# Kernel optimization log

Measured on AMD Instinct MI355X. Metric: run time of the kernel, lower is better.

## Reference

```python
import jax, jax.numpy as jnp
import numpy as np

B, N_LAT, N_CTX, DIM = 4, 512, 4096, 512
HEADS, DIM_HEAD = 8, 64
DIM_INNER = HEADS * DIM_HEAD  # 512


def setup_inputs() -> dict:
    key = jax.random.key(0)
    k1, k2, k3, k4, k5 = jax.random.split(key, 5)
    x = jax.random.normal(k1, (B, N_LAT, DIM), dtype=jnp.float32)
    context = jax.random.normal(k2, (B, N_CTX, DIM), dtype=jnp.float32)
    # eqx.nn.Linear weights have shape (out_features, in_features); scale ~ 1/sqrt(in)
    s = 1.0 / np.sqrt(DIM)
    Wq = jax.random.normal(k3, (DIM_INNER, DIM), dtype=jnp.float32) * s
    Wkv = jax.random.normal(k4, (2 * DIM_INNER, DIM), dtype=jnp.float32) * s
    Wout = jax.random.normal(k5, (DIM, DIM_INNER), dtype=jnp.float32) * (1.0 / np.sqrt(DIM_INNER))
    return {"x": x, "context": context, "Wq": Wq, "Wkv": Wkv, "Wout": Wout}


def reference(x, context, Wq, Wkv, Wout):
    h, d = HEADS, DIM_HEAD
    # queries are prepended to the context (unconditional in the source)
    ctx = jnp.concatenate([x, context], axis=1)              # [b, n+m, dim]
    q = jnp.einsum('bnd,ed->bne', x, Wq)                     # [b, n, h*d]
    kv = jnp.einsum('bmd,ed->bme', ctx, Wkv)                 # [b, n+m, 2*h*d]
    k, v = jnp.split(kv, 2, axis=-1)
    # b n (h d) -> b h n d
    def split_heads(t):
        b, n, _ = t.shape
        return t.reshape(b, n, h, d).transpose(0, 2, 1, 3)
    q, k, v = split_heads(q), split_heads(k), split_heads(v)
    scale = d ** (-0.5)
    scores = jnp.einsum('bhnd,bhmd->bhnm', q, k) * scale     # [b, h, n, n+m]
    attn = jax.nn.softmax(scores, axis=-1)
    out = jnp.einsum('bhnm,bhmd->bhnd', attn, v)             # [b, h, n, d]
    b, _, n, _ = out.shape
    out = out.transpose(0, 2, 1, 3).reshape(b, n, h * d)     # b h n d -> b n (h d)
    return jnp.einsum('bne,de->bnd', out, Wout)
```

## Files before the change

kernel.cpp:

```cpp
#include <hip/hip_runtime.h>
#include <hip/hip_bf16.h>
#include <cstdint>

#define DEVI __device__ __forceinline__

typedef unsigned short u16;
typedef unsigned int u32;
typedef __attribute__((ext_vector_type(8))) short bf16x8;
typedef __attribute__((ext_vector_type(4))) float f32x4;
typedef __attribute__((ext_vector_type(4))) int i32x4;

DEVI u16 f2bf(float f) {
    union { float f; u32 u; } v; v.f = f;
    u32 r = v.u + 0x7fffu + ((v.u >> 16) & 1u);
    return (u16)(r >> 16);
}
DEVI u32 pk2(float a, float b) { return (u32)f2bf(a) | ((u32)f2bf(b) << 16); }

DEVI u32 cvtpk_bf16(float lo, float hi) {
    u32 r;
    asm("v_cvt_pk_bf16_f32 %0, %1, %2" : "=v"(r) : "v"(lo), "v"(hi));
    return r;
}

DEVI void gload_lds16(const void* g, void* l) {
    __builtin_amdgcn_global_load_lds(
        (const __attribute__((address_space(1))) u32*)(uintptr_t)g,
        (__attribute__((address_space(3))) u32*)(u32)(uintptr_t)l,
        16, 0, 0);
}

__global__ __launch_bounds__(256) void prep_all(const float* __restrict__ x,
                                                const float* __restrict__ ctx,
                                                const float* __restrict__ Wq,
                                                const float* __restrict__ Wkv,
                                                const float* __restrict__ Wout,
                                                u16* __restrict__ ctxb,
                                                u16* __restrict__ wqb,
                                                u16* __restrict__ wkvb,
                                                u16* __restrict__ woutb) {
    int id = blockIdx.x;
    int tid = threadIdx.x;
    if (id < 4608) {
        int idx = id * 256 + tid;
        long e0 = (long)idx * 8;
        int b = (int)(e0 / (4608L * 512));
        long rem = e0 % (4608L * 512);
        int m = (int)(rem / 512);
        int d = (int)(rem % 512);
        const float* src = (m < 512) ? (x + ((long)b * 512 + m) * 512 + d)
                                     : (ctx + ((long)b * 4096 + (m - 512)) * 512 + d);
        float4 a = *(const float4*)src;
        float4 c = *(const float4*)(src + 4);
        uint4 u;
        u.x = pk2(a.x, a.y); u.y = pk2(a.z, a.w);
        u.z = pk2(c.x, c.y); u.w = pk2(c.z, c.w);
        *(uint4*)&ctxb[e0] = u;
        return;
    }
    const float* s;
    u16* d;
    int i;
    if (id < 4736)      { s = Wq;   d = wqb;   i = (id - 4608) * 256 + tid; }
    else if (id < 4992) { s = Wkv;  d = wkvb;  i = (id - 4736) * 256 + tid; }
    else                { s = Wout; d = woutb; i = (id - 4992) * 256 + tid; }
    const float4* s4 = (const float4*)s;
    float4 a = s4[i * 2], b = s4[i * 2 + 1];
    uint4 u;
    u.x = pk2(a.x, a.y); u.y = pk2(a.z, a.w);
    u.z = pk2(b.x, b.y); u.w = pk2(b.z, b.w);
    ((uint4*)d)[i] = u;
}

__global__ __launch_bounds__(512) void gemm_kvq(const u16* __restrict__ ctxb,
                                                const u16* __restrict__ wkvb,
                                                const u16* __restrict__ wqb,
                                                u16* __restrict__ kb,
                                                u16* __restrict__ vtb,
                                                u16* __restrict__ qb) {
    const int K = 512;
    __shared__ u16 Asm[2][128 * 64];
    __shared__ u16 Bsm[2][256 * 64];
    int tid = threadIdx.x;
    int w = tid >> 6, l = tid & 63;
    int g = l >> 4, c = l & 15;
    int wr = w >> 2, wc = w & 3;

    const u16* B;
    u16* C;
    long r0, arow0;
    int rpb;
    bool isq = (blockIdx.y >= 144);
    if (isq) {
        if (blockIdx.x >= 2) return;
        r0 = (long)(blockIdx.y - 144) * 128;
        rpb = 512;
        B = wqb;
        C = qb;
    } else {
        r0 = (long)blockIdx.y * 128;
        rpb = 4608;
        B = wkvb;
        C = kb;
    }
    arow0 = (r0 / rpb) * (4608L * 512) + (r0 % rpb) * K;
    int n0 = blockIdx.x * 256;

    f32x4 acc[4][4];
#pragma unroll
    for (int i = 0; i < 4; i++)
#pragma unroll
        for (int j = 0; j < 4; j++) acc[i][j] = (f32x4){0.f, 0.f, 0.f, 0.f};

    int srow = l >> 3;
    int sch = l & 7;

    auto stage = [&](int kt, int bb) {
#pragma unroll
        for (int i = 0; i < 2; i++) {
            int c2 = w * 2 + i;
            int row = c2 * 8 + srow;
            int sc = sch ^ (row & 7);
            gload_lds16(ctxb + arow0 + (long)row * K + kt * 64 + sc * 8,
                        &Asm[bb][c2 * 512 + (l << 3)]);
        }
#pragma unroll
        for (int i = 0; i < 4; i++) {
            int c2 = w * 4 + i;
            int row = c2 * 8 + srow;
            int sc = sch ^ (row & 7);
            gload_lds16(B + (long)(n0 + row) * K + kt * 64 + sc * 8,
                        &Bsm[bb][c2 * 512 + (l << 3)]);
        }
    };

    stage(0, 0);
#pragma unroll 2
    for (int kt = 0; kt < 8; ++kt) {
        int pb = kt & 1;
        if (kt < 7) {
            stage(kt + 1, pb ^ 1);
            asm volatile("s_waitcnt vmcnt(6)" ::: "memory");
        } else {
            asm volatile("s_waitcnt vmcnt(0)" ::: "memory");
        }
        __builtin_amdgcn_s_barrier();
        __builtin_amdgcn_sched_barrier(0);
#pragma unroll
        for (int ks = 0; ks < 2; ++ks) {
            bf16x8 af[4], bfr[4];
#pragma unroll
            for (int mt = 0; mt < 4; ++mt) {
                int row = wr * 64 + mt * 16 + c;
                int ch = (ks * 4 + g) ^ (row & 7);
                af[mt] = *(const bf16x8*)&Asm[pb][row * 64 + ch * 8];
            }
#pragma unroll
            for (int nt = 0; nt < 4; ++nt) {
                int row = wc * 64 + nt * 16 + c;
                int ch = (ks * 4 + g) ^ (row & 7);
                bfr[nt] = *(const bf16x8*)&Bsm[pb][row * 64 + ch * 8];
            }
            __builtin_amdgcn_s_setprio(1);
#pragma unroll
            for (int mt = 0; mt < 4; ++mt)
#pragma unroll
                for (int nt = 0; nt < 4; ++nt)
                    acc[mt][nt] = __builtin_amdgcn_mfma_f32_16x16x32_bf16(
                        af[mt], bfr[nt], acc[mt][nt], 0, 0, 0);
            __builtin_amdgcn_s_setprio(0);
        }
        __builtin_amdgcn_s_barrier();
    }

    if (!isq && n0 >= 512) {
        int b2 = (int)(r0 / 4608);
        int mb = (int)(r0 - (long)b2 * 4608) + wr * 64;
#pragma unroll
        for (int mt = 0; mt < 4; ++mt) {
#pragma unroll
            for (int nt = 0; nt < 4; ++nt) {
                int colv = (n0 - 512) + wc * 64 + nt * 16 + c;
                int hh = colv >> 6, dd = colv & 63;
                long ob = ((long)(b2 * 8 + hh) * 64 + dd) * 4608 + mb
                        + (mt >> 1) * 32 + g * 8 + (mt & 1) * 4;
                ushort4 pk;
                pk.x = f2bf(acc[mt][nt][0]);
                pk.y = f2bf(acc[mt][nt][1]);
                pk.z = f2bf(acc[mt][nt][2]);
                pk.w = f2bf(acc[mt][nt][3]);
                *(ushort4*)&vtb[ob] = pk;
            }
        }
        return;
    }
#pragma unroll
    for (int mt = 0; mt < 4; ++mt) {
#pragma unroll
        for (int r = 0; r < 4; ++r) {
            long row = r0 + wr * 64 + mt * 16 + g * 4 + r;
#pragma unroll
            for (int nt = 0; nt < 4; ++nt) {
                int col = n0 + wc * 64 + nt * 16 + c;
                C[row * 512 + col] = f2bf(acc[mt][nt][r]);
            }
        }
    }
}

__global__ __launch_bounds__(256) void gemm_out(const u16* __restrict__ A,
                                                const u16* __restrict__ B,
                                                float* __restrict__ C) {
    const int K = 512;
    __shared__ u16 Asm[2][64 * 64];
    __shared__ u16 Bsm[2][128 * 64];
    int tid = threadIdx.x;
    int w = tid >> 6, l = tid & 63;
    int g = l >> 4, c = l & 15;
    int wr = w >> 1, wc = w & 1;
    long r0 = (long)blockIdx.y * 64;
    long arow0 = r0 * K;
    int n0 = blockIdx.x * 128;

    f32x4 acc[2][4];
#pragma unroll
    for (int i = 0; i < 2; i++)
#pragma unroll
        for (int j = 0; j < 4; j++) acc[i][j] = (f32x4){0.f, 0.f, 0.f, 0.f};

    int srow = l >> 3;
    int sch = l & 7;

    auto stage = [&](int kt, int bb) {
#pragma unroll
        for (int i = 0; i < 2; i++) {
            int c2 = w * 2 + i;
            int row = c2 * 8 + srow;
            int sc = sch ^ (row & 7);
            gload_lds16(A + arow0 + (long)row * K + kt * 64 + sc * 8,
                        &Asm[bb][c2 * 512 + (l << 3)]);
        }
#pragma unroll
        for (int i = 0; i < 4; i++) {
            int c2 = w * 4 + i;
            int row = c2 * 8 + srow;
            int sc = sch ^ (row & 7);
            gload_lds16(B + (long)(n0 + row) * K + kt * 64 + sc * 8,
                        &Bsm[bb][c2 * 512 + (l << 3)]);
        }
    };

    stage(0, 0);
#pragma unroll 2
    for (int kt = 0; kt < 8; ++kt) {
        int pb = kt & 1;
        if (kt < 7) {
            stage(kt + 1, pb ^ 1);
            asm volatile("s_waitcnt vmcnt(6)" ::: "memory");
        } else {
            asm volatile("s_waitcnt vmcnt(0)" ::: "memory");
        }
        __builtin_amdgcn_s_barrier();
        __builtin_amdgcn_sched_barrier(0);
#pragma unroll
        for (int ks = 0; ks < 2; ++ks) {
            bf16x8 af[2], bfr[4];
#pragma unroll
            for (int mt = 0; mt < 2; ++mt) {
                int row = wr * 32 + mt * 16 + c;
                int ch = (ks * 4 + g) ^ (row & 7);
                af[mt] = *(const bf16x8*)&Asm[pb][row * 64 + ch * 8];
            }
#pragma unroll
            for (int nt = 0; nt < 4; ++nt) {
                int row = wc * 64 + nt * 16 + c;
                int ch = (ks * 4 + g) ^ (row & 7);
                bfr[nt] = *(const bf16x8*)&Bsm[pb][row * 64 + ch * 8];
            }
#pragma unroll
            for (int mt = 0; mt < 2; ++mt)
#pragma unroll
                for (int nt = 0; nt < 4; ++nt)
                    acc[mt][nt] = __builtin_amdgcn_mfma_f32_16x16x32_bf16(
                        af[mt], bfr[nt], acc[mt][nt], 0, 0, 0);
        }
        __builtin_amdgcn_s_barrier();
    }
#pragma unroll
    for (int mt = 0; mt < 2; ++mt) {
#pragma unroll
        for (int r = 0; r < 4; ++r) {
            long row = r0 + wr * 32 + mt * 16 + g * 4 + r;
#pragma unroll
            for (int nt = 0; nt < 4; ++nt) {
                int col = n0 + wc * 64 + nt * 16 + c;
                C[row * 512 + col] = acc[mt][nt][r];
            }
        }
    }
}

__global__ __launch_bounds__(512) void attn_kern(const u16* __restrict__ Q,
                                                 const u16* __restrict__ KB,
                                                 const u16* __restrict__ VT,
                                                 float* __restrict__ Op,
                                                 float2* __restrict__ ML) {
    __shared__ u16 Ksm[2][64 * 64];
    __shared__ u16 Vsm[2][64 * 64];
    int tid = threadIdx.x;
    int w = tid >> 6, l = tid & 63;
    int g = l >> 4, c = l & 15;
    int id = blockIdx.x;
    int u = (id & 7) | ((id >> 5) << 3);
    int qi = (id >> 3) & 3;
    int p_ = u >> 3, chunk = u & 7;
    int b = p_ >> 3, h = p_ & 7;
    int qb0 = qi * 128;
    const int NT = 9;
    int it0 = chunk * NT;

    bf16x8 qf[2];
    {
        long qrow = (long)(b * 512 + qb0 + w * 16 + c);
#pragma unroll
        for (int ks = 0; ks < 2; ++ks)
            qf[ks] = *(const bf16x8*)&Q[qrow * 512 + h * 64 + ks * 32 + g * 8];
    }
    f32x4 o[4];
#pragma unroll
    for (int nt = 0; nt < 4; nt++) o[nt] = (f32x4){0.f, 0.f, 0.f, 0.f};
    float mrun = -1e30f, lrun = 0.f;

    const float SCL = 0.125f * 1.44269504f;
    const long kbase = (long)b * 4608 * 512 + h * 64;
    const long vtbase = (long)(b * 8 + h) * 64 * 4608;

    int srow = tid >> 3;
    int ssc = (tid & 7) ^ (srow & 7);

    auto stage = [&](int it, int bb) {
        gload_lds16(KB + kbase + (long)(it * 64 + srow) * 512 + ssc * 8,
                    &Ksm[bb][tid * 8]);
        gload_lds16(VT + vtbase + (long)srow * 4608 + it * 64 + ssc * 8,
                    &Vsm[bb][tid * 8]);
    };

    stage(it0, 0);
    for (int t = 0; t < NT; ++t) {
        int pbuf = t & 1;
        if (t + 1 < NT) {
            stage(it0 + t + 1, pbuf ^ 1);
            asm volatile("s_waitcnt vmcnt(2)" ::: "memory");
        } else {
            asm volatile("s_waitcnt vmcnt(0)" ::: "memory");
        }
        __builtin_amdgcn_s_barrier();
        __builtin_amdgcn_sched_barrier(0);

        f32x4 st[4];
#pragma unroll
        for (int t2 = 0; t2 < 4; t2++) st[t2] = (f32x4){0.f, 0.f, 0.f, 0.f};
        __builtin_amdgcn_s_setprio(1);
#pragma unroll
        for (int ks = 0; ks < 2; ++ks) {
#pragma unroll
            for (int t2 = 0; t2 < 4; t2++) {
                int row = t2 * 16 + c;
                int ch = (ks * 4 + g) ^ (row & 7);
                bf16x8 kf = *(const bf16x8*)&Ksm[pbuf][row * 64 + ch * 8];
                st[t2] = __builtin_amdgcn_mfma_f32_16x16x32_bf16(kf, qf[ks], st[t2], 0, 0, 0);
            }
        }
        __builtin_amdgcn_s_setprio(0);

        float mx01 = fmaxf(fmaxf(st[0][0], st[0][1]), fmaxf(st[0][2], st[0][3]));
        float mx23 = fmaxf(fmaxf(st[1][0], st[1][1]), fmaxf(st[1][2], st[1][3]));
        float mx45 = fmaxf(fmaxf(st[2][0], st[2][1]), fmaxf(st[2][2], st[2][3]));
        float mx67 = fmaxf(fmaxf(st[3][0], st[3][1]), fmaxf(st[3][2], st[3][3]));
        float mx = fmaxf(fmaxf(mx01, mx23), fmaxf(mx45, mx67)) * SCL;
        mx = fmaxf(mx, __shfl_xor(mx, 16));
        mx = fmaxf(mx, __shfl_xor(mx, 32));

        bool need = mx > mrun + 8.f;
        if (__ballot(need)) {
            float mnew = fmaxf(mrun, mx);
            float rf = exp2f(mrun - mnew);
            mrun = mnew;
            lrun *= rf;
#pragma unroll
            for (int nt = 0; nt < 4; nt++)
#pragma unroll
                for (int r = 0; r < 4; r++) o[nt][r] *= rf;
        }
#pragma unroll
        for (int t2 = 0; t2 < 4; t2++)
#pragma unroll
            for (int r = 0; r < 4; r++) st[t2][r] = exp2f(st[t2][r] * SCL - mrun);

        lrun += ((st[0][0] + st[0][1]) + (st[0][2] + st[0][3]))
              + ((st[1][0] + st[1][1]) + (st[1][2] + st[1][3]))
              + ((st[2][0] + st[2][1]) + (st[2][2] + st[2][3]))
              + ((st[3][0] + st[3][1]) + (st[3][2] + st[3][3]));

        bf16x8 pbf[2];
#pragma unroll
        for (int ks = 0; ks < 2; ++ks) {
            i32x4 vv;
            vv[0] = (int)cvtpk_bf16(st[2 * ks][0], st[2 * ks][1]);
            vv[1] = (int)cvtpk_bf16(st[2 * ks][2], st[2 * ks][3]);
            vv[2] = (int)cvtpk_bf16(st[2 * ks + 1][0], st[2 * ks + 1][1]);
            vv[3] = (int)cvtpk_bf16(st[2 * ks + 1][2], st[2 * ks + 1][3]);
            pbf[ks] = __builtin_bit_cast(bf16x8, vv);
        }

        __builtin_amdgcn_s_setprio(1);
#pragma unroll
        for (int ks = 0; ks < 2; ++ks) {
#pragma unroll
            for (int nt = 0; nt < 4; nt++) {
                int vrow = nt * 16 + c;
                int vch = (ks * 4 + g) ^ (vrow & 7);
                bf16x8 vb = *(const bf16x8*)&Vsm[pbuf][vrow * 64 + vch * 8];
                o[nt] = __builtin_amdgcn_mfma_f32_16x16x32_bf16(vb, pbf[ks], o[nt], 0, 0, 0);
            }
        }
        __builtin_amdgcn_s_setprio(0);
        __builtin_amdgcn_s_barrier();
    }

    lrun += __shfl_xor(lrun, 16);
    lrun += __shfl_xor(lrun, 32);

    long prow = (long)(chunk * 32 + p_) * 512 + qb0 + w * 16;
#pragma unroll
    for (int nt = 0; nt < 4; nt++)
        *(f32x4*)&Op[(prow + c) * 64 + nt * 16 + g * 4] = o[nt];
    if (g == 0) ML[prow + c] = make_float2(mrun, lrun);
}

__global__ __launch_bounds__(256) void attn_combine(const float* __restrict__ Op,
                                                    const float2* __restrict__ ML,
                                                    u16* __restrict__ O) {
    int tid = threadIdx.x;
    int w = tid >> 6, l = tid & 63;
    long rid = (long)blockIdx.x * 4 + w;
    int p_ = (int)(rid >> 9);
    int row = (int)(rid & 511);
    int b = p_ >> 3, h = p_ & 7;
    float2 m[8];
#pragma unroll
    for (int cc = 0; cc < 8; cc++) m[cc] = ML[((long)(cc * 32 + p_) * 512 + row)];
    float mstar = fmaxf(fmaxf(fmaxf(m[0].x, m[1].x), fmaxf(m[2].x, m[3].x)),
                        fmaxf(fmaxf(m[4].x, m[5].x), fmaxf(m[6].x, m[7].x)));
    float wsum = 0.f, acc = 0.f;
#pragma unroll
    for (int cc = 0; cc < 8; cc++) {
        float wgt = exp2f(m[cc].x - mstar);
        wsum += wgt * m[cc].y;
        acc += wgt * Op[((long)(cc * 32 + p_) * 512 + row) * 64 + l];
    }
    O[((long)(b * 512 + row)) * 512 + h * 64 + l] = f2bf(acc / wsum);
}


extern "C" void kernel_launch(void* const* d_in, const int* in_sizes, int n_in,
                              void* d_out, int out_size, void* d_ws, size_t ws_size,
                              hipStream_t stream) {
    const float* x = (const float*)d_in[0];
    const float* ctx = (const float*)d_in[1];
    const float* Wq = (const float*)d_in[2];
    const float* Wkv = (const float*)d_in[3];
    const float* Wout = (const float*)d_in[4];
    float* out = (float*)d_out;

    char* ws = (char*)d_ws;
    size_t off = 0;
    auto alloc = [&](size_t bytes) {
        size_t r = off;
        off += (bytes + 255) & ~(size_t)255;
        return r;
    };
    u16* ctxb = (u16*)(ws + alloc(4L * 4608 * 512 * 2));
    u16* wqb = (u16*)(ws + alloc(512L * 512 * 2));
    u16* wkvb = (u16*)(ws + alloc(1024L * 512 * 2));
    u16* woutb = (u16*)(ws + alloc(512L * 512 * 2));
    u16* qb = (u16*)(ws + alloc(2048L * 512 * 2));
    u16* kb = (u16*)(ws + alloc(4L * 4608 * 512 * 2));
    u16* vtb = (u16*)(ws + alloc(4L * 8 * 64 * 4608 * 2));
    u16* aob = (u16*)(ws + alloc(2048L * 512 * 2));
    float* opb = (float*)(ws + alloc(8L * 32 * 512 * 64 * 4));
    float2* mlb = (float2*)(ws + alloc(8L * 32 * 512 * 8));

    prep_all<<<dim3(5120), dim3(256), 0, stream>>>(x, ctx, Wq, Wkv, Wout,
                                                   ctxb, wqb, wkvb, woutb);
    gemm_kvq<<<dim3(4, 160), dim3(512), 0, stream>>>(ctxb, wkvb, wqb, kb, vtb, qb);
    attn_kern<<<dim3(1024), dim3(512), 0, stream>>>(qb, kb, vtb, opb, mlb);
    attn_combine<<<dim3(4096), dim3(256), 0, stream>>>(opb, mlb, aob);
    gemm_out<<<dim3(4, 32), dim3(256), 0, stream>>>(aob, woutb, out);
}
```

Before: 175.7 us.

## Fold softmax scale into Wq, halve KV GEMM N-tile, sum softmax rows via MFMA

Three separate changes. The attention scale times log2(e) is folded into the bf16 Wq conversion, which removes a per-score multiply in the attention loop. The KV/Q projection GEMM tile shrinks from 128x256 to 128x128 and the grid doubles, giving more blocks and less LDS per block at the cost of reloading the A tile twice as often. The softmax row sum moves from scalar adds and cross-lane shuffles to an extra MFMA against a ones vector, which trades VALU work for matrix-unit work and slightly changes rounding because P is summed in bf16.

```diff
diff --git a/kernel.cpp b/kernel.cpp
--- a/kernel.cpp
+++ b/kernel.cpp
@@ -61,14 +61,16 @@
     const float* s;
     u16* d;
     int i;
-    if (id < 4736)      { s = Wq;   d = wqb;   i = (id - 4608) * 256 + tid; }
+    float scl = 1.0f;
+    if (id < 4736)      { s = Wq;   d = wqb;   i = (id - 4608) * 256 + tid;
+                          scl = 0.125f * 1.44269504f; }
     else if (id < 4992) { s = Wkv;  d = wkvb;  i = (id - 4736) * 256 + tid; }
     else                { s = Wout; d = woutb; i = (id - 4992) * 256 + tid; }
     const float4* s4 = (const float4*)s;
     float4 a = s4[i * 2], b = s4[i * 2 + 1];
     uint4 u;
-    u.x = pk2(a.x, a.y); u.y = pk2(a.z, a.w);
-    u.z = pk2(b.x, b.y); u.w = pk2(b.z, b.w);
+    u.x = pk2(a.x * scl, a.y * scl); u.y = pk2(a.z * scl, a.w * scl);
+    u.z = pk2(b.x * scl, b.y * scl); u.w = pk2(b.z * scl, b.w * scl);
     ((uint4*)d)[i] = u;
 }
 
@@ -80,7 +82,7 @@
                                                 u16* __restrict__ qb) {
     const int K = 512;
     __shared__ u16 Asm[2][128 * 64];
-    __shared__ u16 Bsm[2][256 * 64];
+    __shared__ u16 Bsm[2][128 * 64];
     int tid = threadIdx.x;
     int w = tid >> 6, l = tid & 63;
     int g = l >> 4, c = l & 15;
@@ -89,28 +91,26 @@
     const u16* B;
     u16* C;
     long r0, arow0;
-    int rpb;
     bool isq = (blockIdx.y >= 144);
     if (isq) {
-        if (blockIdx.x >= 2) return;
+        if (blockIdx.x >= 4) return;
         r0 = (long)(blockIdx.y - 144) * 128;
-        rpb = 512;
+        arow0 = (r0 / 512) * (4608L * 512) + (r0 % 512) * K;
         B = wqb;
         C = qb;
     } else {
         r0 = (long)blockIdx.y * 128;
-        rpb = 4608;
+        arow0 = (r0 / 4608) * (4608L * 512) + (r0 % 4608) * K;
         B = wkvb;
         C = kb;
     }
-    arow0 = (r0 / rpb) * (4608L * 512) + (r0 % rpb) * K;
-    int n0 = blockIdx.x * 256;
-
-    f32x4 acc[4][4];
+    int n0 = blockIdx.x * 128;
+
+    f32x4 acc[4][2];
 #pragma unroll
     for (int i = 0; i < 4; i++)
 #pragma unroll
-        for (int j = 0; j < 4; j++) acc[i][j] = (f32x4){0.f, 0.f, 0.f, 0.f};
+        for (int j = 0; j < 2; j++) acc[i][j] = (f32x4){0.f, 0.f, 0.f, 0.f};
 
     int srow = l >> 3;
     int sch = l & 7;
@@ -123,12 +123,6 @@
             int sc = sch ^ (row & 7);
             gload_lds16(ctxb + arow0 + (long)row * K + kt * 64 + sc * 8,
                         &Asm[bb][c2 * 512 + (l << 3)]);
-        }
-#pragma unroll
-        for (int i = 0; i < 4; i++) {
-            int c2 = w * 4 + i;
-            int row = c2 * 8 + srow;
-            int sc = sch ^ (row & 7);
             gload_lds16(B + (long)(n0 + row) * K + kt * 64 + sc * 8,
                         &Bsm[bb][c2 * 512 + (l << 3)]);
         }
@@ -140,7 +134,7 @@
         int pb = kt & 1;
         if (kt < 7) {
             stage(kt + 1, pb ^ 1);
-            asm volatile("s_waitcnt vmcnt(6)" ::: "memory");
+            asm volatile("s_waitcnt vmcnt(4)" ::: "memory");
         } else {
             asm volatile("s_waitcnt vmcnt(0)" ::: "memory");
         }
@@ -148,7 +142,7 @@
         __builtin_amdgcn_sched_barrier(0);
 #pragma unroll
         for (int ks = 0; ks < 2; ++ks) {
-            bf16x8 af[4], bfr[4];
+            bf16x8 af[4], bfr[2];
 #pragma unroll
             for (int mt = 0; mt < 4; ++mt) {
                 int row = wr * 64 + mt * 16 + c;
@@ -156,8 +150,8 @@
                 af[mt] = *(const bf16x8*)&Asm[pb][row * 64 + ch * 8];
             }
 #pragma unroll
-            for (int nt = 0; nt < 4; ++nt) {
-                int row = wc * 64 + nt * 16 + c;
+            for (int nt = 0; nt < 2; ++nt) {
+                int row = wc * 32 + nt * 16 + c;
                 int ch = (ks * 4 + g) ^ (row & 7);
                 bfr[nt] = *(const bf16x8*)&Bsm[pb][row * 64 + ch * 8];
             }
@@ -165,7 +159,7 @@
 #pragma unroll
             for (int mt = 0; mt < 4; ++mt)
 #pragma unroll
-                for (int nt = 0; nt < 4; ++nt)
+                for (int nt = 0; nt < 2; ++nt)
                     acc[mt][nt] = __builtin_amdgcn_mfma_f32_16x16x32_bf16(
                         af[mt], bfr[nt], acc[mt][nt], 0, 0, 0);
             __builtin_amdgcn_s_setprio(0);
@@ -179,8 +173,8 @@
 #pragma unroll
         for (int mt = 0; mt < 4; ++mt) {
 #pragma unroll
-            for (int nt = 0; nt < 4; ++nt) {
-                int colv = (n0 - 512) + wc * 64 + nt * 16 + c;
+            for (int nt = 0; nt < 2; ++nt) {
+                int colv = (n0 - 512) + wc * 32 + nt * 16 + c;
                 int hh = colv >> 6, dd = colv & 63;
                 long ob = ((long)(b2 * 8 + hh) * 64 + dd) * 4608 + mb
                         + (mt >> 1) * 32 + g * 8 + (mt & 1) * 4;
@@ -200,8 +194,8 @@
         for (int r = 0; r < 4; ++r) {
             long row = r0 + wr * 64 + mt * 16 + g * 4 + r;
 #pragma unroll
-            for (int nt = 0; nt < 4; ++nt) {
-                int col = n0 + wc * 64 + nt * 16 + c;
+            for (int nt = 0; nt < 2; ++nt) {
+                int col = n0 + wc * 32 + nt * 16 + c;
                 C[row * 512 + col] = f2bf(acc[mt][nt][r]);
             }
         }
@@ -326,12 +320,16 @@
         for (int ks = 0; ks < 2; ++ks)
             qf[ks] = *(const bf16x8*)&Q[qrow * 512 + h * 64 + ks * 32 + g * 8];
     }
+    bf16x8 onesf;
+#pragma unroll
+    for (int e = 0; e < 8; e++) onesf[e] = (short)0x3F80;
+
     f32x4 o[4];
 #pragma unroll
     for (int nt = 0; nt < 4; nt++) o[nt] = (f32x4){0.f, 0.f, 0.f, 0.f};
-    float mrun = -1e30f, lrun = 0.f;
-
-    const float SCL = 0.125f * 1.44269504f;
+    f32x4 ls = (f32x4){0.f, 0.f, 0.f, 0.f};
+    float mrun = -1e30f;
+
     const long kbase = (long)b * 4608 * 512 + h * 64;
     const long vtbase = (long)(b * 8 + h) * 64 * 4608;
 
@@ -377,7 +375,7 @@
         float mx23 = fmaxf(fmaxf(st[1][0], st[1][1]), fmaxf(st[1][2], st[1][3]));
         float mx45 = fmaxf(fmaxf(st[2][0], st[2][1]), fmaxf(st[2][2], st[2][3]));
         float mx67 = fmaxf(fmaxf(st[3][0], st[3][1]), fmaxf(st[3][2], st[3][3]));
-        float mx = fmaxf(fmaxf(mx01, mx23), fmaxf(mx45, mx67)) * SCL;
+        float mx = fmaxf(fmaxf(mx01, mx23), fmaxf(mx45, mx67));
         mx = fmaxf(mx, __shfl_xor(mx, 16));
         mx = fmaxf(mx, __shfl_xor(mx, 32));
 
@@ -386,7 +384,8 @@
             float mnew = fmaxf(mrun, mx);
             float rf = exp2f(mrun - mnew);
             mrun = mnew;
-            lrun *= rf;
+#pragma unroll
+            for (int r = 0; r < 4; r++) ls[r] *= rf;
 #pragma unroll
             for (int nt = 0; nt < 4; nt++)
 #pragma unroll
@@ -395,12 +394,7 @@
 #pragma unroll
         for (int t2 = 0; t2 < 4; t2++)
 #pragma unroll
-            for (int r = 0; r < 4; r++) st[t2][r] = exp2f(st[t2][r] * SCL - mrun);
-
-        lrun += ((st[0][0] + st[0][1]) + (st[0][2] + st[0][3]))
-              + ((st[1][0] + st[1][1]) + (st[1][2] + st[1][3]))
-              + ((st[2][0] + st[2][1]) + (st[2][2] + st[2][3]))
-              + ((st[3][0] + st[3][1]) + (st[3][2] + st[3][3]));
+            for (int r = 0; r < 4; r++) st[t2][r] = exp2f(st[t2][r] - mrun);
 
         bf16x8 pbf[2];
 #pragma unroll
@@ -416,6 +410,7 @@
         __builtin_amdgcn_s_setprio(1);
 #pragma unroll
         for (int ks = 0; ks < 2; ++ks) {
+            ls = __builtin_amdgcn_mfma_f32_16x16x32_bf16(onesf, pbf[ks], ls, 0, 0, 0);
 #pragma unroll
             for (int nt = 0; nt < 4; nt++) {
                 int vrow = nt * 16 + c;
@@ -428,14 +423,11 @@
         __builtin_amdgcn_s_barrier();
     }
 
-    lrun += __shfl_xor(lrun, 16);
-    lrun += __shfl_xor(lrun, 32);
-
     long prow = (long)(chunk * 32 + p_) * 512 + qb0 + w * 16;
 #pragma unroll
     for (int nt = 0; nt < 4; nt++)
         *(f32x4*)&Op[(prow + c) * 64 + nt * 16 + g * 4] = o[nt];
-    if (g == 0) ML[prow + c] = make_float2(mrun, lrun);
+    if (g == 0) ML[prow + c] = make_float2(mrun, ls[0]);
 }
 
 __global__ __launch_bounds__(256) void attn_combine(const float* __restrict__ Op,
@@ -493,7 +485,7 @@
 
     prep_all<<<dim3(5120), dim3(256), 0, stream>>>(x, ctx, Wq, Wkv, Wout,
                                                    ctxb, wqb, wkvb, woutb);
-    gemm_kvq<<<dim3(4, 160), dim3(512), 0, stream>>>(ctxb, wkvb, wqb, kb, vtb, qb);
+    gemm_kvq<<<dim3(8, 160), dim3(512), 0, stream>>>(ctxb, wkvb, wqb, kb, vtb, qb);
     attn_kern<<<dim3(1024), dim3(512), 0, stream>>>(qb, kb, vtb, opb, mlb);
     attn_combine<<<dim3(4096), dim3(256), 0, stream>>>(opb, mlb, aob);
     gemm_out<<<dim3(4, 32), dim3(256), 0, stream>>>(aob, woutb, out);
```

Result: no change. 174.5 us (-0.6%).
